# Kernel optimization log

Measured on AMD Instinct MI355X. Metric: run time of the kernel, lower is better.

The kernel has to match this reference:

```python
import jax, jax.numpy as jnp
import numpy as np

ACTION_NS = [3, 3, 2, 4, 24]        # forward_back, left_right, jump, sneak_sprint, attack_...
RANGE_STARTS = [6, 8, 10, 11, 14]   # action_ranges starts (indices 0..5 are commit + camera ops)
N_ACTIONS = 37
LOGIT_DIM = 36
MIN_DELTA = 0.5 / 2**3
MAX_STEP = 20
MAX_CAMSTEP = 6
B, NUM_INPUT, HIDDEN = 32768, 1024, 2048
D_IN = NUM_INPUT + 4 + LOGIT_DIM


def setup_inputs():
    key = jax.random.key(0)
    ks = jax.random.split(key, 12)
    inp = {
        "fc_input": jax.random.normal(ks[0], (B, NUM_INPUT), jnp.float32),
        "camera": jax.random.normal(ks[1], (B, 2), jnp.float32),
        "rand_u": jax.random.uniform(ks[2], (B,), jnp.float32),
        "W1": (jax.random.normal(ks[3], (D_IN, HIDDEN), jnp.float32) / np.sqrt(D_IN)).astype(jnp.float32),
        "b1": jnp.zeros((HIDDEN,), jnp.float32),
        "W2": (jax.random.normal(ks[4], (HIDDEN, N_ACTIONS), jnp.float32) / np.sqrt(HIDDEN)).astype(jnp.float32),
        "b2": jnp.zeros((N_ACTIONS,), jnp.float32),
    }
    names = ["act_fb", "act_lr", "act_jp", "act_ss", "act_atk"]
    for i, (nm, n) in enumerate(zip(names, ACTION_NS)):
        inp[nm] = jax.random.randint(ks[5 + i], (B,), 0, n, jnp.int32)
    return inp


def _discretize_scan(camera, acts):
    # Faithful jax version of the 20-step no_grad target/input construction loop.
    nB = camera.shape[0]
    cam0, cam1 = camera[:, 0], camera[:, 1]

    def step(carry, _):
        ac, delta, rdac, dch, cam_steps, committed, norm = carry
        oh = [jax.nn.one_hot(r, n, dtype=jnp.float32) for r, n in zip(rdac, ACTION_NS)]
        inp_vec = jnp.concatenate([ac] + oh + [delta[:, None], dch.astype(jnp.float32)[:, None]], axis=1)  # [B,40]
        norm = norm + (~committed).astype(jnp.float32)
        commit = ((jnp.abs(cam0) < 1e-5) & (jnp.abs(cam1) < 1e-5)) | (cam_steps >= MAX_CAMSTEP)
        for r, a in zip(rdac, acts):
            commit = commit & (r == a)
        dac = jnp.zeros((nB,), jnp.int32)
        modified = commit
        new_rdac = []
        for r, a, rs in zip(rdac, acts, RANGE_STARTS):
            disc = (~modified) & (r != a)
            dac = jnp.where(disc & (a == 0), r - 1 + rs, jnp.where(disc, a - 1 + rs, dac))
            new_rdac.append(jnp.where(disc, a, r))
            modified = modified | disc
        d2 = delta * 2.0
        # NOTE: original torch code compares cam[:,1] against ac[:,0]; bug preserved.
        dmask = (~modified) & (~dch) & ((jnp.abs(cam0 - ac[:, 0]) > d2) | (jnp.abs(cam1 - ac[:, 0]) > d2))
        dac = jnp.where(dmask, 5, dac)
        delta = jnp.where(dmask, jnp.clip(d2, -0.5, 0.5), delta)
        modified = modified | dmask
        sx = jnp.where(cam0 < ac[:, 0], -1.0, 1.0)
        sy = jnp.where(cam1 < ac[:, 1], -1.0, 1.0)
        quad = jnp.where(sx < 0, jnp.where(sy < 0, 1, 3), jnp.where(sy < 0, 2, 4)).astype(jnp.int32)
        dac = jnp.where(~modified, quad, dac)
        move = jnp.stack([sx, sy], axis=1) * delta[:, None]
        ac = jnp.where((~modified)[:, None], ac + move, ac)
        delta = jnp.where(~modified, delta * 0.5, delta)
        dch = dch | (~modified)
        cam_steps = cam_steps + (~modified).astype(jnp.int32)
        committed = committed | commit
        return (ac, delta, tuple(new_rdac), dch, cam_steps, committed, norm), (inp_vec, dac)

    init = (jnp.zeros((nB, 2), jnp.float32),
            jnp.full((nB,), MIN_DELTA, jnp.float32),
            tuple(jnp.zeros((nB,), jnp.int32) for _ in ACTION_NS),
            jnp.zeros((nB,), bool),
            jnp.zeros((nB,), jnp.int32),
            jnp.zeros((nB,), bool),
            jnp.zeros((nB,), jnp.float32))
    carry, (all_inputs, all_dacs) = jax.lax.scan(step, init, None, length=MAX_STEP)
    return all_inputs, all_dacs, carry[-1]  # [T,B,40], [T,B], norm [B]


def reference(fc_input, camera, rand_u, W1, b1, W2, b2, act_fb, act_lr, act_jp, act_ss, act_atk):
    acts = (act_fb, act_lr, act_jp, act_ss, act_atk)
    all_inputs, all_dacs, norm = _discretize_scan(camera, acts)
    rand_sam = jnp.minimum((rand_u * norm).astype(jnp.int32), MAX_STEP - 1)  # sample an uncommitted step
    idx = jnp.arange(fc_input.shape[0])
    sel = jax.lax.stop_gradient(all_inputs[rand_sam, idx])  # [B,40]
    tgt = jax.lax.stop_gradient(all_dacs[rand_sam, idx])    # [B]
    x = jnp.concatenate([fc_input, sel], axis=1)
    h = x @ W1 + b1
    h = h * jax.nn.sigmoid(h)  # swish
    logits = h @ W2 + b2
    logp = jax.nn.log_softmax(logits, axis=-1)
    loss = -jnp.take_along_axis(logp, tgt[:, None], axis=1)[:, 0]  # per-sample CE (reduction='none')
    return loss
```

## Files before the change

### kernel.cpp

```cpp
#include <hip/hip_runtime.h>
#include <hip/hip_bf16.h>
#include <stdint.h>

#define B_ROWS 32768
#define NUM_IN 1024
#define D_PAD2 1152
#define HID    2048
#define NPAD   64

typedef __attribute__((ext_vector_type(8))) short bf16x8;
typedef __attribute__((ext_vector_type(4))) float f32x4;
typedef unsigned short ushort_t;

__device__ __forceinline__ unsigned short f2bf(float f){
  union { float f; uint32_t u; } x; x.f = f;
  uint32_t u = x.u;
  return (unsigned short)((u + 0x7FFFu + ((u >> 16) & 1u)) >> 16);
}

__device__ __forceinline__ void gload16(const void* g, void* l){
  __builtin_amdgcn_global_load_lds((const __attribute__((address_space(1))) void*)g,
                                   (__attribute__((address_space(3))) void*)l, 16, 0, 0);
}

__device__ __forceinline__ int disc_step(
    float cam0, float cam1, const int a[5],
    float& ac0, float& ac1, float& delta,
    int r[5], bool& dch, int& cam_steps, bool& committed, float& norm)
{
  const int RS[5] = {6, 8, 10, 11, 14};
  norm += committed ? 0.0f : 1.0f;
  bool commit = ((fabsf(cam0) < 1e-5f) && (fabsf(cam1) < 1e-5f)) || (cam_steps >= 6);
  #pragma unroll
  for (int i = 0; i < 5; ++i) commit = commit && (r[i] == a[i]);
  int dac = 0;
  bool modified = commit;
  #pragma unroll
  for (int i = 0; i < 5; ++i){
    bool disc = (!modified) && (r[i] != a[i]);
    if (disc){
      dac = (a[i] == 0) ? (r[i] - 1 + RS[i]) : (a[i] - 1 + RS[i]);
      r[i] = a[i];
      modified = true;
    }
  }
  float d2 = delta * 2.0f;
  bool dmask = (!modified) && (!dch) &&
               ((fabsf(cam0 - ac0) > d2) || (fabsf(cam1 - ac0) > d2));
  if (dmask){ dac = 5; delta = fminf(d2, 0.5f); modified = true; }
  if (!modified){
    float sx = (cam0 < ac0) ? -1.0f : 1.0f;
    float sy = (cam1 < ac1) ? -1.0f : 1.0f;
    dac = (sx < 0.0f) ? ((sy < 0.0f) ? 1 : 3) : ((sy < 0.0f) ? 2 : 4);
    ac0 += sx * delta; ac1 += sy * delta;
    delta *= 0.5f;
    dch = true;
    cam_steps += 1;
  }
  committed = committed || commit;
  return dac;
}

__global__ void k_disc(const float* __restrict__ camera, const float* __restrict__ rand_u,
                       const int* __restrict__ afb, const int* __restrict__ alr,
                       const int* __restrict__ ajp, const int* __restrict__ ass,
                       const int* __restrict__ aat,
                       unsigned short* __restrict__ xb, int* __restrict__ tgt)
{
  int row = blockIdx.x * 256 + threadIdx.x;
  if (row >= B_ROWS) return;
  float cam0 = camera[2*row], cam1 = camera[2*row + 1];
  int a[5] = { afb[row], alr[row], ajp[row], ass[row], aat[row] };

  float ac0 = 0.f, ac1 = 0.f, delta = 0.0625f, norm = 0.f;
  int r[5] = {0,0,0,0,0};
  bool dch = false, committed = false; int cam_steps = 0;
  for (int t = 0; t < 20; ++t)
    disc_step(cam0, cam1, a, ac0, ac1, delta, r, dch, cam_steps, committed, norm);

  int rs = (int)(rand_u[row] * norm);
  if (rs > 19) rs = 19;
  if (rs < 0) rs = 0;

  ac0 = 0.f; ac1 = 0.f; delta = 0.0625f; norm = 0.f;
  r[0]=r[1]=r[2]=r[3]=r[4]=0; dch = false; committed = false; cam_steps = 0;
  for (int t = 0; t < rs; ++t)
    disc_step(cam0, cam1, a, ac0, ac1, delta, r, dch, cam_steps, committed, norm);

  float vec[40];
  #pragma unroll
  for (int j = 0; j < 40; ++j) vec[j] = 0.0f;
  vec[0] = ac0; vec[1] = ac1;
  const int offs[5] = {2, 5, 8, 10, 14};
  #pragma unroll
  for (int i = 0; i < 5; ++i) vec[offs[i] + r[i]] = 1.0f;
  vec[38] = delta; vec[39] = dch ? 1.0f : 0.0f;

  int dac = disc_step(cam0, cam1, a, ac0, ac1, delta, r, dch, cam_steps, committed, norm);
  tgt[row] = dac;

  unsigned short* o = xb + (size_t)row * D_PAD2 + NUM_IN;
  #pragma unroll
  for (int j = 0; j < 40; ++j) o[j] = f2bf(vec[j]);
  for (int j = 40; j < D_PAD2 - NUM_IN; ++j) o[j] = 0;
}

__global__ void k_fc(const float* __restrict__ fc, unsigned short* __restrict__ xb)
{
  int gid = blockIdx.x * 256 + threadIdx.x;
  int row = gid >> 7;
  int c   = gid & 127;
  const float4* p = (const float4*)(fc + (size_t)row * NUM_IN + c * 8);
  float4 f0 = p[0], f1 = p[1];
  unsigned short o[8] = { f2bf(f0.x), f2bf(f0.y), f2bf(f0.z), f2bf(f0.w),
                          f2bf(f1.x), f2bf(f1.y), f2bf(f1.z), f2bf(f1.w) };
  uint4 pk;
  pk.x = (uint32_t)o[0] | ((uint32_t)o[1] << 16);
  pk.y = (uint32_t)o[2] | ((uint32_t)o[3] << 16);
  pk.z = (uint32_t)o[4] | ((uint32_t)o[5] << 16);
  pk.w = (uint32_t)o[6] | ((uint32_t)o[7] << 16);
  *(uint4*)(xb + (size_t)row * D_PAD2 + c * 8) = pk;
}

__global__ void k_w1t(const float* __restrict__ W1, unsigned short* __restrict__ w1t)
{
  int idx = blockIdx.x * 256 + threadIdx.x;
  if (idx >= HID * D_PAD2) return;
  int n = idx / D_PAD2;
  int k = idx - n * D_PAD2;
  float v = (k < 1064) ? W1[(size_t)k * HID + n] : 0.0f;
  w1t[idx] = f2bf(v);
}

__global__ void k_w2t(const float* __restrict__ W2, unsigned short* __restrict__ w2t)
{
  int idx = blockIdx.x * 256 + threadIdx.x;
  if (idx >= NPAD * HID) return;
  int n = idx >> 11;
  int k = idx & (HID - 1);
  float v = (n < 37) ? W2[(size_t)k * 37 + n] : 0.0f;
  w2t[idx] = f2bf(v);
}

#define LDS_A0 0
#define LDS_A1 16384
#define LDS_B0 32768
#define LDS_B1 49152

#define STAGE(G, REG, ROW0, KT, HALF) do { \
    const ushort_t* s0_ = (G) + (size_t)((ROW0) + (HALF)*128 + srow) * D_PAD2 + ((KT) << 6) + scol; \
    gload16(s0_, lds + (REG) + (HALF)*8192 + t*8); \
    gload16(s0_ + (size_t)64 * D_PAD2, lds + (REG) + (HALF)*8192 + 4096 + t*8); \
  } while(0)

#define LDA_(REG, MH) do { \
    _Pragma("unroll") for (int mi_ = 0; mi_ < 4; ++mi_){ \
      const int row_ = arow_base + (MH)*64 + mi_*16; \
      _Pragma("unroll") for (int kk_ = 0; kk_ < 2; ++kk_) \
        aR[mi_][kk_] = *(const bf16x8*)(lds + (REG) + row_*64 + (((kk_*4+lg)^axor)<<3)); \
    } \
  } while(0)

#define LDB_(REG, NH, BR) do { \
    _Pragma("unroll") for (int ni_ = 0; ni_ < 2; ++ni_){ \
      const int row_ = brow_base + (NH)*32 + ni_*16; \
      _Pragma("unroll") for (int kk_ = 0; kk_ < 2; ++kk_) \
        BR[ni_][kk_] = *(const bf16x8*)(lds + (REG) + row_*64 + (((kk_*4+lg)^axor)<<3)); \
    } \
  } while(0)

#define MMA(MH, NH, BR) do { \
    __builtin_amdgcn_s_setprio(1); \
    _Pragma("unroll") for (int mi_ = 0; mi_ < 4; ++mi_) \
    _Pragma("unroll") for (int ni_ = 0; ni_ < 2; ++ni_) \
    _Pragma("unroll") for (int kk_ = 0; kk_ < 2; ++kk_) \
      acc[(MH)*4+mi_][(NH)*2+ni_] = __builtin_amdgcn_mfma_f32_16x16x32_bf16( \
          aR[mi_][kk_], BR[ni_][kk_], acc[(MH)*4+mi_][(NH)*2+ni_], 0, 0, 0); \
    __builtin_amdgcn_s_setprio(0); \
  } while(0)

#define BAR() __builtin_amdgcn_s_barrier()
#define WAIT_LGKM0() asm volatile("s_waitcnt lgkmcnt(0)" ::: "memory")
#define WAIT_VM6()   asm volatile("s_waitcnt vmcnt(6)" ::: "memory")

__global__ __launch_bounds__(512, 2) void k_gemm1(const ushort_t* __restrict__ xb,
                                                  const ushort_t* __restrict__ w1t,
                                                  const float* __restrict__ b1,
                                                  ushort_t* __restrict__ hb)
{
  __shared__ ushort_t lds[65536];
  const int t = threadIdx.x;
  const int lane = t & 63;
  const int wid = t >> 6, wm = wid >> 2, wn = wid & 3;
  const int lr = lane & 15, lg = lane >> 4;

  const int bid = blockIdx.x;
  const int swz = (bid & 7) * 128 + (bid >> 3);
  const int brow = (swz >> 3) << 8;
  const int bcol = (swz & 7) << 8;

  const int srow = t >> 3;
  const int scol = ((t & 7) ^ (srow & 7)) << 3;

  const int axor = lr & 7;
  const int arow_base = wm*128 + lr;
  const int brow_base = wn*64 + lr;

  f32x4 acc[8][4] = {};
  bf16x8 aR[4][2], bR0[2][2], bR1[2][2];

  STAGE(xb,  LDS_A0, brow, 0, 0);  STAGE(xb,  LDS_A0, brow, 0, 1);
  STAGE(w1t, LDS_B0, bcol, 0, 0);  STAGE(w1t, LDS_B0, bcol, 0, 1);
  STAGE(w1t, LDS_B1, bcol, 1, 0);  STAGE(w1t, LDS_B1, bcol, 1, 1);
  STAGE(xb,  LDS_A1, brow, 1, 0);
  WAIT_VM6();
  BAR();

  for (int i = 0; i < 9; ++i){
    const int c1 = 2*i + 1;
    const int n0 = (2*i + 2 <= 17) ? 2*i + 2 : 16;
    const int n1 = (2*i + 3 <= 17) ? 2*i + 3 : 17;

    LDA_(LDS_A0, 0); LDB_(LDS_B0, 0, bR0); LDB_(LDS_B0, 1, bR1);
    STAGE(xb, LDS_A1, brow, c1, 1);
    BAR(); WAIT_LGKM0();
    MMA(0, 0, bR0);
    BAR();
    STAGE(w1t, LDS_B0, bcol, n0, 0);
    BAR();
    MMA(0, 1, bR1);
    BAR();
    LDA_(LDS_A0, 1);
    STAGE(w1t, LDS_B0, bcol, n0, 1);
    BAR(); WAIT_LGKM0();
    MMA(1, 0, bR0);
    BAR();
    STAGE(xb, LDS_A0, brow, n0, 0);
    WAIT_VM6();
    BAR();
    MMA(1, 1, bR1);
    BAR();
    LDA_(LDS_A1, 0); LDB_(LDS_B1, 0, bR0); LDB_(LDS_B1, 1, bR1);
    STAGE(xb, LDS_A0, brow, n0, 1);
    BAR(); WAIT_LGKM0();
    MMA(0, 0, bR0);
    BAR();
    STAGE(w1t, LDS_B1, bcol, n1, 0);
    BAR();
    MMA(0, 1, bR1);
    BAR();
    LDA_(LDS_A1, 1);
    STAGE(w1t, LDS_B1, bcol, n1, 1);
    BAR(); WAIT_LGKM0();
    MMA(1, 0, bR0);
    BAR();
    STAGE(xb, LDS_A1, brow, n1, 0);
    WAIT_VM6();
    BAR();
    MMA(1, 1, bR1);
    BAR();
  }

  #pragma unroll
  for (int ni = 0; ni < 4; ++ni){
    const int col = bcol + wn*64 + ni*16 + lr;
    const float bias = b1[col];
    #pragma unroll
    for (int mi = 0; mi < 8; ++mi){
      #pragma unroll
      for (int i2 = 0; i2 < 4; ++i2){
        const int row = brow + wm*128 + mi*16 + lg*4 + i2;
        float v = acc[mi][ni][i2] + bias;
        float s = v / (1.0f + __expf(-v));
        hb[(size_t)row * HID + col] = f2bf(s);
      }
    }
  }
}

__global__ __launch_bounds__(256) void k_gemm2(const unsigned short* __restrict__ hb,
                                               const unsigned short* __restrict__ w2t,
                                               const float* __restrict__ b2,
                                               const int* __restrict__ tgt,
                                               float* __restrict__ loss)
{
  __shared__ __align__(16) unsigned short As[128 * 64];
  __shared__ __align__(16) unsigned short Bs[64 * 64];
  const int t = threadIdx.x;
  const int lane = t & 63, wid = t >> 6;
  const int lr = lane & 15, lg = lane >> 4;
  const int row0 = blockIdx.x * 128;
  f32x4 acc[2][4] = {};

  for (int kt = 0; kt < HID / 64; ++kt){
    const int k0 = kt * 64;
    #pragma unroll
    for (int i = 0; i < 4; ++i){
      int c = i * 256 + t, r = c >> 3, cc = c & 7;
      gload16(hb + (size_t)(row0 + r) * HID + k0 + cc * 8, As + c * 8);
    }
    #pragma unroll
    for (int i = 0; i < 2; ++i){
      int c = i * 256 + t, r = c >> 3, cc = c & 7;
      gload16(w2t + (size_t)r * HID + k0 + cc * 8, Bs + c * 8);
    }
    __syncthreads();
    #pragma unroll
    for (int kk = 0; kk < 2; ++kk){
      bf16x8 a[2], b[4];
      #pragma unroll
      for (int mi = 0; mi < 2; ++mi)
        a[mi] = *(const bf16x8*)(As + (wid*32 + mi*16 + lr) * 64 + kk*32 + lg*8);
      #pragma unroll
      for (int ni = 0; ni < 4; ++ni)
        b[ni] = *(const bf16x8*)(Bs + (ni*16 + lr) * 64 + kk*32 + lg*8);
      #pragma unroll
      for (int mi = 0; mi < 2; ++mi)
        #pragma unroll
        for (int ni = 0; ni < 4; ++ni)
          acc[mi][ni] = __builtin_amdgcn_mfma_f32_16x16x32_bf16(a[mi], b[ni], acc[mi][ni], 0, 0, 0);
    }
    __syncthreads();
  }

  float bias_n[4];
  #pragma unroll
  for (int ni = 0; ni < 4; ++ni){
    int col = ni*16 + lr;
    bias_n[ni] = (col < 37) ? b2[col] : 0.0f;
  }

  #pragma unroll
  for (int mi = 0; mi < 2; ++mi){
    #pragma unroll
    for (int i2 = 0; i2 < 4; ++i2){
      const int row = row0 + wid*32 + mi*16 + lg*4 + i2;
      float v[4]; float m = -1e30f;
      #pragma unroll
      for (int ni = 0; ni < 4; ++ni){
        int col = ni*16 + lr;
        float x = (col < 37) ? (acc[mi][ni][i2] + bias_n[ni]) : -1e30f;
        v[ni] = x; m = fmaxf(m, x);
      }
      #pragma unroll
      for (int off = 1; off < 16; off <<= 1) m = fmaxf(m, __shfl_xor(m, off, 64));
      float se = 0.0f;
      #pragma unroll
      for (int ni = 0; ni < 4; ++ni) se += __expf(v[ni] - m);
      #pragma unroll
      for (int off = 1; off < 16; off <<= 1) se += __shfl_xor(se, off, 64);
      const int tg = tgt[row];
      float pick = 0.0f;
      #pragma unroll
      for (int ni = 0; ni < 4; ++ni){
        int col = ni*16 + lr;
        pick += (col == tg) ? v[ni] : 0.0f;
      }
      #pragma unroll
      for (int off = 1; off < 16; off <<= 1) pick += __shfl_xor(pick, off, 64);
      if (lr == 0) loss[row] = m + __logf(se) - pick;
    }
  }
}

extern "C" void kernel_launch(void* const* d_in, const int* in_sizes, int n_in,
                              void* d_out, int out_size, void* d_ws, size_t ws_size,
                              hipStream_t stream)
{
  (void)in_sizes; (void)n_in; (void)out_size; (void)ws_size;
  const float* fc  = (const float*)d_in[0];
  const float* cam = (const float*)d_in[1];
  const float* ru  = (const float*)d_in[2];
  const float* W1  = (const float*)d_in[3];
  const float* b1  = (const float*)d_in[4];
  const float* W2  = (const float*)d_in[5];
  const float* b2  = (const float*)d_in[6];
  const int* afb = (const int*)d_in[7];
  const int* alr = (const int*)d_in[8];
  const int* ajp = (const int*)d_in[9];
  const int* ass = (const int*)d_in[10];
  const int* aat = (const int*)d_in[11];
  float* loss = (float*)d_out;

  char* ws = (char*)d_ws;
  unsigned short* xb  = (unsigned short*)(ws);
  unsigned short* w1t = (unsigned short*)(ws + 75497472);
  unsigned short* w2t = (unsigned short*)(ws + 80216064);
  int*            tgt = (int*)           (ws + 80478208);
  unsigned short* hb  = (unsigned short*)(ws + 80609280);

  k_fc  <<<16384, 256, 0, stream>>>(fc, xb);
  k_w1t <<<(HID * D_PAD2 + 255) / 256, 256, 0, stream>>>(W1, w1t);
  k_w2t <<<(NPAD * HID + 255) / 256, 256, 0, stream>>>(W2, w2t);
  k_disc<<<(B_ROWS + 255) / 256, 256, 0, stream>>>(cam, ru, afb, alr, ajp, ass, aat, xb, tgt);

  k_gemm1<<<(B_ROWS/256) * (HID/256), 512, 0, stream>>>(xb, w1t, b1, hb);
  k_gemm2<<<B_ROWS / 128, 256, 0, stream>>>(hb, w2t, b2, tgt, loss);
}
```

Measured before the change: 275.0 us.

## Fuse second GEMM into first GEMM epilogue with split-K partial logits

The swish activations from the first GEMM are staged into swizzled LDS instead of being written to global memory as bf16. Each block then multiplies its 256-column slice by W2 to produce partial logits, which go to an fp32 buffer with one slab per column block. A new reduction kernel sums the eight partials and applies bias, log-softmax and target pick. This drops the 128MB hidden write and reread, but adds a 64MB fp32 partial buffer and extra epilogue work inside the GEMM1 blocks.

```diff
diff --git a/kernel.cpp b/kernel.cpp
--- a/kernel.cpp
+++ b/kernel.cpp
@@ -182,11 +182,13 @@
 #define BAR() __builtin_amdgcn_s_barrier()
 #define WAIT_LGKM0() asm volatile("s_waitcnt lgkmcnt(0)" ::: "memory")
 #define WAIT_VM6()   asm volatile("s_waitcnt vmcnt(6)" ::: "memory")
+#define WAIT_VM0()   asm volatile("s_waitcnt vmcnt(0)" ::: "memory")
 
 __global__ __launch_bounds__(512, 2) void k_gemm1(const ushort_t* __restrict__ xb,
                                                   const ushort_t* __restrict__ w1t,
+                                                  const ushort_t* __restrict__ w2t,
                                                   const float* __restrict__ b1,
-                                                  ushort_t* __restrict__ hb)
+                                                  float* __restrict__ pbuf)
 {
   __shared__ ushort_t lds[65536];
   const int t = threadIdx.x;
@@ -261,105 +263,87 @@
     BAR();
   }
 
-  #pragma unroll
-  for (int ni = 0; ni < 4; ++ni){
-    const int col = bcol + wn*64 + ni*16 + lr;
-    const float bias = b1[col];
-    #pragma unroll
-    for (int mi = 0; mi < 8; ++mi){
+  WAIT_VM0();
+  BAR();
+
+  float b1v[4];
+  #pragma unroll
+  for (int ni = 0; ni < 4; ++ni) b1v[ni] = b1[bcol + wn*64 + ni*16 + lr];
+
+  #pragma unroll
+  for (int mi = 0; mi < 8; ++mi){
+    #pragma unroll
+    for (int ni = 0; ni < 4; ++ni){
+      const int col = wn*64 + ni*16 + lr;
       #pragma unroll
       for (int i2 = 0; i2 < 4; ++i2){
-        const int row = brow + wm*128 + mi*16 + lg*4 + i2;
-        float v = acc[mi][ni][i2] + bias;
+        const int row = wm*128 + mi*16 + lg*4 + i2;
+        float v = acc[mi][ni][i2] + b1v[ni];
         float s = v / (1.0f + __expf(-v));
-        hb[(size_t)row * HID + col] = f2bf(s);
+        const int chunk = (col >> 3) ^ (row & 7);
+        lds[row*256 + chunk*8 + (col & 7)] = f2bf(s);
       }
     }
   }
-}
-
-__global__ __launch_bounds__(256) void k_gemm2(const unsigned short* __restrict__ hb,
-                                               const unsigned short* __restrict__ w2t,
-                                               const float* __restrict__ b2,
-                                               const int* __restrict__ tgt,
-                                               float* __restrict__ loss)
-{
-  __shared__ __align__(16) unsigned short As[128 * 64];
-  __shared__ __align__(16) unsigned short Bs[64 * 64];
-  const int t = threadIdx.x;
-  const int lane = t & 63, wid = t >> 6;
-  const int lr = lane & 15, lg = lane >> 4;
-  const int row0 = blockIdx.x * 128;
-  f32x4 acc[2][4] = {};
-
-  for (int kt = 0; kt < HID / 64; ++kt){
-    const int k0 = kt * 64;
-    #pragma unroll
-    for (int i = 0; i < 4; ++i){
-      int c = i * 256 + t, r = c >> 3, cc = c & 7;
-      gload16(hb + (size_t)(row0 + r) * HID + k0 + cc * 8, As + c * 8);
+  __syncthreads();
+
+  const int rb = wid * 32;
+  f32x4 acc2[2][4] = {};
+  #pragma unroll
+  for (int ks = 0; ks < 8; ++ks){
+    bf16x8 a2[2], b2f[4];
+    #pragma unroll
+    for (int m = 0; m < 2; ++m){
+      const int row = rb + m*16 + lr;
+      a2[m] = *(const bf16x8*)(lds + row*256 + (((ks*4+lg) ^ (lr & 7)) << 3));
     }
     #pragma unroll
-    for (int i = 0; i < 2; ++i){
-      int c = i * 256 + t, r = c >> 3, cc = c & 7;
-      gload16(w2t + (size_t)r * HID + k0 + cc * 8, Bs + c * 8);
-    }
-    __syncthreads();
-    #pragma unroll
-    for (int kk = 0; kk < 2; ++kk){
-      bf16x8 a[2], b[4];
-      #pragma unroll
-      for (int mi = 0; mi < 2; ++mi)
-        a[mi] = *(const bf16x8*)(As + (wid*32 + mi*16 + lr) * 64 + kk*32 + lg*8);
+    for (int ni = 0; ni < 4; ++ni)
+      b2f[ni] = *(const bf16x8*)(w2t + (size_t)(ni*16 + lr) * HID + bcol + ks*32 + lg*8);
+    #pragma unroll
+    for (int m = 0; m < 2; ++m)
       #pragma unroll
       for (int ni = 0; ni < 4; ++ni)
-        b[ni] = *(const bf16x8*)(Bs + (ni*16 + lr) * 64 + kk*32 + lg*8);
+        acc2[m][ni] = __builtin_amdgcn_mfma_f32_16x16x32_bf16(a2[m], b2f[ni], acc2[m][ni], 0, 0, 0);
+  }
+
+  const int cb = bcol >> 8;
+  #pragma unroll
+  for (int m = 0; m < 2; ++m)
+    #pragma unroll
+    for (int ni = 0; ni < 4; ++ni)
       #pragma unroll
-      for (int mi = 0; mi < 2; ++mi)
-        #pragma unroll
-        for (int ni = 0; ni < 4; ++ni)
-          acc[mi][ni] = __builtin_amdgcn_mfma_f32_16x16x32_bf16(a[mi], b[ni], acc[mi][ni], 0, 0, 0);
-    }
-    __syncthreads();
-  }
-
-  float bias_n[4];
-  #pragma unroll
-  for (int ni = 0; ni < 4; ++ni){
-    int col = ni*16 + lr;
-    bias_n[ni] = (col < 37) ? b2[col] : 0.0f;
-  }
-
-  #pragma unroll
-  for (int mi = 0; mi < 2; ++mi){
-    #pragma unroll
-    for (int i2 = 0; i2 < 4; ++i2){
-      const int row = row0 + wid*32 + mi*16 + lg*4 + i2;
-      float v[4]; float m = -1e30f;
-      #pragma unroll
-      for (int ni = 0; ni < 4; ++ni){
-        int col = ni*16 + lr;
-        float x = (col < 37) ? (acc[mi][ni][i2] + bias_n[ni]) : -1e30f;
-        v[ni] = x; m = fmaxf(m, x);
+      for (int i2 = 0; i2 < 4; ++i2){
+        const int r = brow + rb + m*16 + lg*4 + i2;
+        pbuf[((size_t)cb << 21) + ((size_t)r << 6) + ni*16 + lr] = acc2[m][ni][i2];
       }
-      #pragma unroll
-      for (int off = 1; off < 16; off <<= 1) m = fmaxf(m, __shfl_xor(m, off, 64));
-      float se = 0.0f;
-      #pragma unroll
-      for (int ni = 0; ni < 4; ++ni) se += __expf(v[ni] - m);
-      #pragma unroll
-      for (int off = 1; off < 16; off <<= 1) se += __shfl_xor(se, off, 64);
-      const int tg = tgt[row];
-      float pick = 0.0f;
-      #pragma unroll
-      for (int ni = 0; ni < 4; ++ni){
-        int col = ni*16 + lr;
-        pick += (col == tg) ? v[ni] : 0.0f;
-      }
-      #pragma unroll
-      for (int off = 1; off < 16; off <<= 1) pick += __shfl_xor(pick, off, 64);
-      if (lr == 0) loss[row] = m + __logf(se) - pick;
-    }
+}
+
+__global__ __launch_bounds__(256) void k_red(const float* __restrict__ pbuf,
+                                             const float* __restrict__ b2,
+                                             const int* __restrict__ tgt,
+                                             float* __restrict__ loss)
+{
+  const int lane = threadIdx.x & 63, w = threadIdx.x >> 6;
+  const int row0 = blockIdx.x * 128 + w * 32;
+  const float bias = (lane < 37) ? b2[lane] : 0.0f;
+  for (int i = 0; i < 32; ++i){
+    const int r = row0 + i;
+    float s = 0.0f;
+    #pragma unroll
+    for (int cb = 0; cb < 8; ++cb)
+      s += pbuf[((size_t)cb << 21) + ((size_t)r << 6) + lane];
+    float x = (lane < 37) ? (s + bias) : -1e30f;
+    float m = x;
+    #pragma unroll
+    for (int off = 1; off < 64; off <<= 1) m = fmaxf(m, __shfl_xor(m, off, 64));
+    float e = __expf(x - m);
+    float se = e;
+    #pragma unroll
+    for (int off = 1; off < 64; off <<= 1) se += __shfl_xor(se, off, 64);
+    const int tg = tgt[r];
+    const float pick = __shfl(x, tg, 64);
+    if (lane == 0) loss[r] = m + __logf(se) - pick;
   }
 }
 
@@ -387,13 +371,13 @@
   unsigned short* w1t = (unsigned short*)(ws + 75497472);
   unsigned short* w2t = (unsigned short*)(ws + 80216064);
   int*            tgt = (int*)           (ws + 80478208);
-  unsigned short* hb  = (unsigned short*)(ws + 80609280);
+  float*          pbuf= (float*)         (ws + 80609280);
 
   k_fc  <<<16384, 256, 0, stream>>>(fc, xb);
   k_w1t <<<(HID * D_PAD2 + 255) / 256, 256, 0, stream>>>(W1, w1t);
   k_w2t <<<(NPAD * HID + 255) / 256, 256, 0, stream>>>(W2, w2t);
   k_disc<<<(B_ROWS + 255) / 256, 256, 0, stream>>>(cam, ru, afb, alr, ajp, ass, aat, xb, tgt);
 
-  k_gemm1<<<(B_ROWS/256) * (HID/256), 512, 0, stream>>>(xb, w1t, b1, hb);
-  k_gemm2<<<B_ROWS / 128, 256, 0, stream>>>(hb, w2t, b2, tgt, loss);
-}
+  k_gemm1<<<(B_ROWS/256) * (HID/256), 512, 0, stream>>>(xb, w1t, w2t, b1, pbuf);
+  k_red  <<<B_ROWS / 128, 256, 0, stream>>>(pbuf, b2, tgt, loss);
+}
```

New measurement: 284.1 us. +3.3%, slower.
